# Optimization experiments

Hardware: AMD Instinct MI355X
Metric: run time of the kernel (lower is better)

The kernel has to match this reference:

```python
import jax, jax.numpy as jnp
import numpy as np

B, S, H = 8, 512, 768
NH, DH = 12, 64
I = 3072
E = 8
TOPK = 2
EPS = 1e-12


def _ln(x, g, b):
    m = jnp.mean(x, axis=-1, keepdims=True)
    v = jnp.mean(jnp.square(x - m), axis=-1, keepdims=True)
    return (x - m) * jax.lax.rsqrt(v + EPS) * g + b


def setup_inputs() -> dict:
    key = jax.random.key(0)
    ks = jax.random.split(key, 20)
    s_h = 1.0 / np.sqrt(H)
    s_i = 1.0 / np.sqrt(I)
    inp = {
        "hidden_states": jax.random.normal(ks[0], (B, S, H), jnp.float32),
        "Wq": jax.random.normal(ks[1], (H, H), jnp.float32) * s_h,
        "bq": jnp.zeros((H,), jnp.float32),
        "Wk": jax.random.normal(ks[2], (H, H), jnp.float32) * s_h,
        "bk": jnp.zeros((H,), jnp.float32),
        "Wv": jax.random.normal(ks[3], (H, H), jnp.float32) * s_h,
        "bv": jnp.zeros((H,), jnp.float32),
        "Wo": jax.random.normal(ks[4], (H, H), jnp.float32) * s_h,
        "bo": jnp.zeros((H,), jnp.float32),
        "ln_attn_g": jnp.ones((H,), jnp.float32),
        "ln_attn_b": jnp.zeros((H,), jnp.float32),
        "ln_ffn_g": jnp.ones((H,), jnp.float32),
        "ln_ffn_b": jnp.zeros((H,), jnp.float32),
        "Wr": jax.random.normal(ks[5], (H, E), jnp.float32) * s_h,
        "br": jnp.zeros((E,), jnp.float32),
        "W_up": jax.random.normal(ks[6], (E, H, I), jnp.float32) * s_h,
        "b_up": jnp.zeros((E, I), jnp.float32),
        "W_new": jax.random.normal(ks[7], (E, H, I), jnp.float32) * s_h,
        "b_new": jnp.zeros((E, I), jnp.float32),
        "W_down": jax.random.normal(ks[8], (E, I, H), jnp.float32) * s_i,
        "b_down": jnp.zeros((E, H), jnp.float32),
    }
    return inp


def reference(hidden_states, Wq, bq, Wk, bk, Wv, bv, Wo, bo,
              ln_attn_g, ln_attn_b, ln_ffn_g, ln_ffn_b,
              Wr, br, W_up, b_up, W_new, b_new, W_down, b_down):
    x = hidden_states
    # --- BertSelfAttention ---
    q = (x @ Wq + bq).reshape(B, S, NH, DH).transpose(0, 2, 1, 3)
    k = (x @ Wk + bk).reshape(B, S, NH, DH).transpose(0, 2, 1, 3)
    v = (x @ Wv + bv).reshape(B, S, NH, DH).transpose(0, 2, 1, 3)
    scores = jnp.einsum("bhqd,bhkd->bhqk", q, k) / np.sqrt(DH)
    probs = jax.nn.softmax(scores, axis=-1)
    ctx = jnp.einsum("bhqk,bhkd->bhqd", probs, v)
    ctx = ctx.transpose(0, 2, 1, 3).reshape(B, S, H)
    # --- BertSelfOutput: dense + residual + LayerNorm ---
    attention_output = _ln(ctx @ Wo + bo + x, ln_attn_g, ln_attn_b)
    # --- feed_forward_chunk: LayerNorm then token top-k MoE ---
    xl = _ln(attention_output, ln_ffn_g, ln_ffn_b)
    router_logits = xl @ Wr + br                      # [B,S,E]
    router_probs = jax.nn.softmax(router_logits, axis=-1)
    topw, topi = jax.lax.top_k(router_probs, TOPK)    # [B,S,K]
    topw = topw / jnp.sum(topw, axis=-1, keepdims=True)
    gates = jnp.sum(jax.nn.one_hot(topi, E, dtype=xl.dtype) * topw[..., None], axis=-2)  # [B,S,E]
    # --- experts (BertExpert: gelu(up(x)) * new(x) -> down), dense over E ---
    up = jax.nn.gelu(jnp.einsum("bsh,ehi->ebsi", xl, W_up) + b_up[:, None, None, :], approximate=False)
    gate_h = jnp.einsum("bsh,ehi->ebsi", xl, W_new) + b_new[:, None, None, :]
    y = jnp.einsum("ebsi,eih->ebsh", up * gate_h, W_down) + b_down[:, None, None, :]
    moe_out = jnp.einsum("ebsh,bse->bsh", y, gates)
    layer_output = moe_out + attention_output
    return layer_output, router_logits
```

## Files before the change

### kernel.cpp

```cpp
#include <hip/hip_runtime.h>
#include <hip/hip_bf16.h>
#include <cmath>


constexpr int cB = 8, cS = 512, cH = 768, cNH = 12, cDH = 64, cI = 3072, cE = 8;
constexpr int cT = cB * cS;
constexpr size_t TH = (size_t)cT * cH;

typedef __hip_bfloat16 bf16;
typedef __attribute__((ext_vector_type(8))) short s8v;
typedef __attribute__((ext_vector_type(4))) float f4v;

constexpr size_t SZ_WEXP     = (size_t)cE * cI * cH / 2;
constexpr size_t OFF_WUP_T   = 0;
constexpr size_t OFF_WNEW_T  = OFF_WUP_T + SZ_WEXP;
constexpr size_t OFF_WDOWN_T = OFF_WNEW_T + SZ_WEXP;
constexpr size_t OFF_QKV     = OFF_WDOWN_T + SZ_WEXP;
constexpr size_t OFF_CTX     = OFF_QKV + 4 * TH;
constexpr size_t OFF_XLB     = OFF_CTX + TH;
constexpr size_t OFF_WGT     = OFF_XLB + TH / 2;
constexpr size_t OFF_COUNTS  = OFF_WGT + 2 * cT;
constexpr size_t OFF_LISTS   = OFF_COUNTS + 16;

__device__ __forceinline__ void glds16(const void* g, void* l) {
    __builtin_amdgcn_global_load_lds(
        (const __attribute__((address_space(1))) unsigned int*)g,
        (__attribute__((address_space(3))) unsigned int*)l, 16, 0, 0);
}

__global__ void init_counts_kernel(int* __restrict__ counts) {
    if (threadIdx.x < cE) counts[threadIdx.x] = 0;
}

__global__ __launch_bounds__(256) void transpose_bf16_kernel(
    const float* __restrict__ src, bf16* __restrict__ dst, int R, int C) {
    __shared__ float tile[64][65];
    const size_t zb = (size_t)blockIdx.z * R * C;
    const int r0 = blockIdx.y * 64, c0 = blockIdx.x * 64;
    const int t = threadIdx.x;
    const int lr = t >> 4, lc = (t & 15) * 4;
#pragma unroll
    for (int i = 0; i < 4; ++i) {
        float4 v = *(const float4*)(src + zb + (size_t)(r0 + lr + i * 16) * C + c0 + lc);
        tile[lr + i * 16][lc + 0] = v.x; tile[lr + i * 16][lc + 1] = v.y;
        tile[lr + i * 16][lc + 2] = v.z; tile[lr + i * 16][lc + 3] = v.w;
    }
    __syncthreads();
#pragma unroll
    for (int i = 0; i < 4; ++i) {
        int cr = lr + i * 16;
        bf16 o[4];
#pragma unroll
        for (int j = 0; j < 4; ++j) o[j] = (bf16)tile[lc + j][cr];
        *(uint2*)(dst + zb + (size_t)(c0 + cr) * R + r0 + lc) = *(uint2*)o;
    }
}

__device__ __forceinline__ void gemm_body128(
    const float* __restrict__ A, const float* __restrict__ B,
    const float* __restrict__ bias, float* __restrict__ C,
    int N, int K, int m0, int n0) {
    __shared__ float As[16 * 132];
    __shared__ float Bs[16 * 128];
    const int t = threadIdx.x;
    const int tx = t & 15, ty = t >> 4;
    const int ar = t >> 2, ac = (t & 3) * 4;
    const int bc = (t & 31) * 4, br = t >> 5;
    const float* gB0 = B + (size_t)br * N + n0 + bc;
    float* dB0 = Bs + t * 4;
    float acc[8][8] = {};
    for (int k0 = 0; k0 < K; k0 += 16) {
        float4 a0 = *(const float4*)(A + (size_t)(m0 + ar) * K + k0 + ac);
        float4 a1 = *(const float4*)(A + (size_t)(m0 + ar + 64) * K + k0 + ac);
        glds16(gB0, dB0);
        glds16(gB0 + (size_t)8 * N, dB0 + 1024);
        As[(ac + 0) * 132 + ar] = a0.x; As[(ac + 1) * 132 + ar] = a0.y;
        As[(ac + 2) * 132 + ar] = a0.z; As[(ac + 3) * 132 + ar] = a0.w;
        As[(ac + 0) * 132 + ar + 64] = a1.x; As[(ac + 1) * 132 + ar + 64] = a1.y;
        As[(ac + 2) * 132 + ar + 64] = a1.z; As[(ac + 3) * 132 + ar + 64] = a1.w;
        __syncthreads();
#pragma unroll
        for (int kk = 0; kk < 16; ++kk) {
            float a[8], b[8];
            *(float4*)&a[0] = *(const float4*)&As[kk * 132 + ty * 8];
            *(float4*)&a[4] = *(const float4*)&As[kk * 132 + ty * 8 + 4];
            *(float4*)&b[0] = *(const float4*)&Bs[kk * 128 + tx * 4];
            *(float4*)&b[4] = *(const float4*)&Bs[kk * 128 + tx * 4 + 64];
#pragma unroll
            for (int i = 0; i < 8; ++i)
#pragma unroll
                for (int j = 0; j < 8; ++j) acc[i][j] += a[i] * b[j];
        }
        __syncthreads();
        gB0 += (size_t)16 * N;
    }
#pragma unroll
    for (int i = 0; i < 8; ++i) {
        int m = m0 + ty * 8 + i;
        float4 o0, o1;
        o0.x = acc[i][0] + bias[n0 + tx * 4 + 0];
        o0.y = acc[i][1] + bias[n0 + tx * 4 + 1];
        o0.z = acc[i][2] + bias[n0 + tx * 4 + 2];
        o0.w = acc[i][3] + bias[n0 + tx * 4 + 3];
        o1.x = acc[i][4] + bias[n0 + 64 + tx * 4 + 0];
        o1.y = acc[i][5] + bias[n0 + 64 + tx * 4 + 1];
        o1.z = acc[i][6] + bias[n0 + 64 + tx * 4 + 2];
        o1.w = acc[i][7] + bias[n0 + 64 + tx * 4 + 3];
        *(float4*)(C + (size_t)m * N + n0 + tx * 4) = o0;
        *(float4*)(C + (size_t)m * N + n0 + 64 + tx * 4) = o1;
    }
}

__global__ __launch_bounds__(256) void gemm_qkv_kernel(
    const float* __restrict__ A,
    const float* __restrict__ Wq, const float* __restrict__ Wk,
    const float* __restrict__ Wv,
    const float* __restrict__ bq, const float* __restrict__ bk,
    const float* __restrict__ bv,
    float* __restrict__ q, float* __restrict__ k, float* __restrict__ v) {
    const int z = blockIdx.z;
    const float* B = (z == 0) ? Wq : (z == 1) ? Wk : Wv;
    const float* bias = (z == 0) ? bq : (z == 1) ? bk : bv;
    float* C = (z == 0) ? q : (z == 1) ? k : v;
    gemm_body128(A, B, bias, C, cH, cH, blockIdx.y * 128, blockIdx.x * 128);
}

__global__ __launch_bounds__(256) void gemm_bias_kernel(
    const float* __restrict__ A, const float* __restrict__ B,
    const float* __restrict__ bias, float* __restrict__ C,
    int M, int N, int K) {
    gemm_body128(A, B, bias, C, N, K, blockIdx.y * 128, blockIdx.x * 128);
}

__global__ __launch_bounds__(256) void attn_kernel(
    const float* __restrict__ q, const float* __restrict__ k,
    const float* __restrict__ v, float* __restrict__ ctx) {
    __shared__ float sQ[64][68];
    __shared__ float sKV[64][68];
    __shared__ float sS[64][68];
    __shared__ float sM[64], sL[64], sAl[64];
    const int q0 = blockIdx.x * 64, h = blockIdx.y, b = blockIdx.z;
    const int t = threadIdx.x;
    const int lr = t >> 2, lq = (t & 3) * 16;
    {
        const float* gq = q + (size_t)(b * cS + q0 + lr) * cH + h * cDH + lq;
#pragma unroll
        for (int j = 0; j < 4; ++j) {
            float4 x = *(const float4*)(gq + j * 4);
            x.x *= 0.125f; x.y *= 0.125f; x.z *= 0.125f; x.w *= 0.125f;
            *(float4*)&sQ[lr][lq + j * 4] = x;
        }
    }
    if (t < 64) { sM[t] = -1e30f; sL[t] = 0.f; }
    const int c0 = t & 15, rr = (t >> 4) * 4;
    const int d4 = (t & 15) * 4, rp = (t >> 4) * 4;
    const int sr = t >> 2, sc = (t & 3) * 16;
    float4 o_acc[4];
#pragma unroll
    for (int i = 0; i < 4; ++i) o_acc[i] = make_float4(0.f, 0.f, 0.f, 0.f);

    for (int kt = 0; kt < 8; ++kt) {
        float4 kreg[4];
        {
            const float* gk = k + (size_t)(b * cS + kt * 64 + lr) * cH + h * cDH + lq;
#pragma unroll
            for (int j = 0; j < 4; ++j) kreg[j] = *(const float4*)(gk + j * 4);
        }
        __syncthreads();
#pragma unroll
        for (int j = 0; j < 4; ++j) *(float4*)&sKV[lr][lq + j * 4] = kreg[j];
        __syncthreads();
        float accS[4][4] = {};
#pragma unroll
        for (int d = 0; d < 64; d += 4) {
            float4 qv[4], kv[4];
#pragma unroll
            for (int i = 0; i < 4; ++i) qv[i] = *(const float4*)&sQ[rr + i][d];
#pragma unroll
            for (int j = 0; j < 4; ++j) kv[j] = *(const float4*)&sKV[c0 + 16 * j][d];
#pragma unroll
            for (int i = 0; i < 4; ++i)
#pragma unroll
                for (int j = 0; j < 4; ++j)
                    accS[i][j] += qv[i].x * kv[j].x + qv[i].y * kv[j].y +
                                  qv[i].z * kv[j].z + qv[i].w * kv[j].w;
        }
#pragma unroll
        for (int i = 0; i < 4; ++i)
#pragma unroll
            for (int j = 0; j < 4; ++j) sS[rr + i][c0 + 16 * j] = accS[i][j];
        float4 vreg[4];
        {
            const float* gv = v + (size_t)(b * cS + kt * 64 + lr) * cH + h * cDH + lq;
#pragma unroll
            for (int j = 0; j < 4; ++j) vreg[j] = *(const float4*)(gv + j * 4);
        }
        __syncthreads();
        {
            float4 s[4];
#pragma unroll
            for (int j = 0; j < 4; ++j) s[j] = *(const float4*)&sS[sr][sc + j * 4];
            float m = -1e30f;
#pragma unroll
            for (int j = 0; j < 4; ++j)
                m = fmaxf(m, fmaxf(fmaxf(s[j].x, s[j].y), fmaxf(s[j].z, s[j].w)));
            m = fmaxf(m, __shfl_xor(m, 1));
            m = fmaxf(m, __shfl_xor(m, 2));
            float m_old = sM[sr];
            float m_new = fmaxf(m_old, m);
            float sum = 0.f;
#pragma unroll
            for (int j = 0; j < 4; ++j) {
                s[j].x = __expf(s[j].x - m_new); s[j].y = __expf(s[j].y - m_new);
                s[j].z = __expf(s[j].z - m_new); s[j].w = __expf(s[j].w - m_new);
                sum += s[j].x + s[j].y + s[j].z + s[j].w;
                *(float4*)&sS[sr][sc + j * 4] = s[j];
            }
            sum += __shfl_xor(sum, 1);
            sum += __shfl_xor(sum, 2);
            if ((t & 3) == 0) {
                float alpha = __expf(m_old - m_new);
                sAl[sr] = alpha;
                sM[sr] = m_new;
                sL[sr] = sL[sr] * alpha + sum;
            }
        }
#pragma unroll
        for (int j = 0; j < 4; ++j) *(float4*)&sKV[lr][lq + j * 4] = vreg[j];
        __syncthreads();
#pragma unroll
        for (int i = 0; i < 4; ++i) {
            float al = sAl[rp + i];
            o_acc[i].x *= al; o_acc[i].y *= al; o_acc[i].z *= al; o_acc[i].w *= al;
        }
        for (int kk4 = 0; kk4 < 64; kk4 += 4) {
            float4 pv[4], vv[4];
#pragma unroll
            for (int i = 0; i < 4; ++i) pv[i] = *(const float4*)&sS[rp + i][kk4];
#pragma unroll
            for (int j = 0; j < 4; ++j) vv[j] = *(const float4*)&sKV[kk4 + j][d4];
#pragma unroll
            for (int i = 0; i < 4; ++i) {
                o_acc[i].x += pv[i].x * vv[0].x + pv[i].y * vv[1].x +
                              pv[i].z * vv[2].x + pv[i].w * vv[3].x;
                o_acc[i].y += pv[i].x * vv[0].y + pv[i].y * vv[1].y +
                              pv[i].z * vv[2].y + pv[i].w * vv[3].y;
                o_acc[i].z += pv[i].x * vv[0].z + pv[i].y * vv[1].z +
                              pv[i].z * vv[2].z + pv[i].w * vv[3].z;
                o_acc[i].w += pv[i].x * vv[0].w + pv[i].y * vv[1].w +
                              pv[i].z * vv[2].w + pv[i].w * vv[3].w;
            }
        }
    }
    __syncthreads();
#pragma unroll
    for (int i = 0; i < 4; ++i) {
        float inv = 1.0f / sL[rp + i];
        float4 o = o_acc[i];
        o.x *= inv; o.y *= inv; o.z *= inv; o.w *= inv;
        *(float4*)(ctx + (size_t)(b * cS + q0 + rp + i) * cH + h * cDH + d4) = o;
    }
}

__device__ __forceinline__ float block_reduce_sum(float v, float* red) {
#pragma unroll
    for (int o = 32; o; o >>= 1) v += __shfl_xor(v, o);
    __syncthreads();
    if ((threadIdx.x & 63) == 0) red[threadIdx.x >> 6] = v;
    __syncthreads();
    return red[0] + red[1] + red[2] + red[3];
}

__global__ __launch_bounds__(256) void ln_router_kernel(
    const float* __restrict__ dense, const float* __restrict__ resid,
    const float* __restrict__ g1, const float* __restrict__ b1,
    const float* __restrict__ g2, const float* __restrict__ b2,
    const float* __restrict__ Wr, const float* __restrict__ br,
    float* __restrict__ out, bf16* __restrict__ xlb,
    float* __restrict__ out_logits, float* __restrict__ wgt,
    int* __restrict__ counts, int* __restrict__ lists) {
    __shared__ float red[4];
    __shared__ float lred[4][8];
    const int t = blockIdx.x, tid = threadIdx.x;
    const size_t base = (size_t)t * cH;
    float v[3], s = 0.f;
#pragma unroll
    for (int i = 0; i < 3; ++i) {
        v[i] = dense[base + tid + 256 * i] + resid[base + tid + 256 * i];
        s += v[i];
    }
    const float mean = block_reduce_sum(s, red) * (1.0f / cH);
    float vs = 0.f;
#pragma unroll
    for (int i = 0; i < 3; ++i) { float d = v[i] - mean; vs += d * d; }
    const float rstd = rsqrtf(block_reduce_sum(vs, red) * (1.0f / cH) + 1e-12f);
    float a[3], s2 = 0.f;
#pragma unroll
    for (int i = 0; i < 3; ++i) {
        a[i] = (v[i] - mean) * rstd * g1[tid + 256 * i] + b1[tid + 256 * i];
        out[base + tid + 256 * i] = a[i];
        s2 += a[i];
    }
    const float mean2 = block_reduce_sum(s2, red) * (1.0f / cH);
    float vs2 = 0.f;
#pragma unroll
    for (int i = 0; i < 3; ++i) { float d = a[i] - mean2; vs2 += d * d; }
    const float rstd2 = rsqrtf(block_reduce_sum(vs2, red) * (1.0f / cH) + 1e-12f);
    float xl[3];
#pragma unroll
    for (int i = 0; i < 3; ++i) {
        xl[i] = (a[i] - mean2) * rstd2 * g2[tid + 256 * i] + b2[tid + 256 * i];
        xlb[base + tid + 256 * i] = (bf16)xl[i];
    }
    float lg[cE] = {};
#pragma unroll
    for (int i = 0; i < 3; ++i) {
        const float* wr = Wr + (size_t)(tid + 256 * i) * cE;
#pragma unroll
        for (int e = 0; e < cE; ++e) lg[e] += xl[i] * wr[e];
    }
#pragma unroll
    for (int e = 0; e < cE; ++e)
#pragma unroll
        for (int o = 32; o; o >>= 1) lg[e] += __shfl_xor(lg[e], o);
    if ((tid & 63) == 0)
#pragma unroll
        for (int e = 0; e < cE; ++e) lred[tid >> 6][e] = lg[e];
    __syncthreads();
    if (tid == 0) {
        float logits[cE];
#pragma unroll
        for (int e = 0; e < cE; ++e) {
            logits[e] = lred[0][e] + lred[1][e] + lred[2][e] + lred[3][e] + br[e];
            out_logits[(size_t)t * cE + e] = logits[e];
        }
        int i0 = 0;
        for (int e = 1; e < cE; ++e) if (logits[e] > logits[i0]) i0 = e;
        int i1 = (i0 == 0) ? 1 : 0;
        for (int e = 0; e < cE; ++e)
            if (e != i0 && logits[e] > logits[i1]) i1 = e;
        float e1 = __expf(logits[i1] - logits[i0]);
        float w0 = 1.0f / (1.0f + e1);
        float w1 = e1 * w0;
        wgt[t * 2 + 0] = w0;
        wgt[t * 2 + 1] = w1;
        int p0 = atomicAdd(&counts[i0], 1);
        lists[i0 * cT + p0] = t * 2 + 0;
        int p1 = atomicAdd(&counts[i1], 1);
        lists[i1 * cT + p1] = t * 2 + 1;
    }
}

__global__ __launch_bounds__(256) void expert_up_mfma_kernel(
    const bf16* __restrict__ xlb,
    const bf16* __restrict__ WupT, const bf16* __restrict__ WnewT,
    const float* __restrict__ b_up, const float* __restrict__ b_new,
    const int* __restrict__ counts, const int* __restrict__ lists,
    bf16* __restrict__ act) {
    const int e = blockIdx.z;
    const int cnt = counts[e];
    const int m0 = blockIdx.y * 128;
    if (m0 >= cnt) return;
    const int n0 = blockIdx.x * 64;
    __shared__ short sA[128 * 32], sB1[64 * 32], sB2[64 * 32];
    __shared__ int rowa[128];
    const int t = threadIdx.x;
    if (t < 128) {
        int idx = m0 + t;
        rowa[t] = (idx < cnt) ? lists[e * cT + idx] : -1;
    }
    __syncthreads();
    const int lane = t & 63, w = t >> 6;
    const int wm = (w >> 1) * 64, wn = (w & 1) * 32;
    const int rA0 = t >> 2, kc8 = (t & 3) * 8;
    int a0 = rowa[rA0], a1 = rowa[rA0 + 64];
    const bf16* gA0 = xlb + (size_t)(a0 < 0 ? 0 : (a0 >> 1)) * cH + kc8;
    const bf16* gA1 = xlb + (size_t)(a1 < 0 ? 0 : (a1 >> 1)) * cH + kc8;
    const bf16* B1 = WupT + (size_t)e * cI * cH;
    const bf16* B2 = WnewT + (size_t)e * cI * cH;
    const bf16* gB1 = B1 + (size_t)(n0 + rA0) * cH + kc8;
    const bf16* gB2 = B2 + (size_t)(n0 + rA0) * cH + kc8;
    short* dA0 = sA + t * 8;   short* dA1 = sA + (t + 256) * 8;
    short* dB1 = sB1 + t * 8;  short* dB2 = sB2 + t * 8;
    f4v zero = {0.f, 0.f, 0.f, 0.f};
    f4v acc1[4][2], acc2[4][2];
#pragma unroll
    for (int i = 0; i < 4; ++i)
#pragma unroll
        for (int j = 0; j < 2; ++j) { acc1[i][j] = zero; acc2[i][j] = zero; }
    const int fr = lane & 15, kg = (lane >> 4) * 8;
    for (int kk = 0; kk < cH; kk += 32) {
        glds16(gA0, dA0); glds16(gA1, dA1);
        glds16(gB1, dB1); glds16(gB2, dB2);
        __syncthreads();
        s8v af[4], bf1[2], bf2[2];
#pragma unroll
        for (int i = 0; i < 4; ++i)
            af[i] = *(const s8v*)(sA + (wm + i * 16 + fr) * 32 + kg);
#pragma unroll
        for (int j = 0; j < 2; ++j) {
            bf1[j] = *(const s8v*)(sB1 + (wn + j * 16 + fr) * 32 + kg);
            bf2[j] = *(const s8v*)(sB2 + (wn + j * 16 + fr) * 32 + kg);
        }
#pragma unroll
        for (int mi = 0; mi < 4; ++mi)
#pragma unroll
            for (int ni = 0; ni < 2; ++ni) {
                acc1[mi][ni] = __builtin_amdgcn_mfma_f32_16x16x32_bf16(
                    af[mi], bf1[ni], acc1[mi][ni], 0, 0, 0);
                acc2[mi][ni] = __builtin_amdgcn_mfma_f32_16x16x32_bf16(
                    af[mi], bf2[ni], acc2[mi][ni], 0, 0, 0);
            }
        __syncthreads();
        gA0 += 32; gA1 += 32; gB1 += 32; gB2 += 32;
    }
    const int cn = lane & 15, rq = (lane >> 4) * 4;
#pragma unroll
    for (int mi = 0; mi < 4; ++mi)
#pragma unroll
        for (int r = 0; r < 4; ++r) {
            int ml = wm + mi * 16 + rq + r;
            int a = rowa[ml];
            if (a < 0) continue;
            bf16* orow = act + (size_t)a * cI + n0 + wn;
#pragma unroll
            for (int ni = 0; ni < 2; ++ni) {
                int nl = ni * 16 + cn;
                float up = acc1[mi][ni][r] + b_up[e * cI + n0 + wn + nl];
                float nw = acc2[mi][ni][r] + b_new[e * cI + n0 + wn + nl];
                float g = 0.5f * up * (1.0f + erff(up * 0.70710678118654752f));
                orow[nl] = (bf16)(g * nw);
            }
        }
}

__global__ __launch_bounds__(256) void expert_down_mfma_kernel(
    const bf16* __restrict__ act, const bf16* __restrict__ WdownT,
    const float* __restrict__ b_down,
    const int* __restrict__ counts, const int* __restrict__ lists,
    const float* __restrict__ wgt, float* __restrict__ out) {
    const int e = blockIdx.z;
    const int cnt = counts[e];
    const int m0 = blockIdx.y * 128;
    if (m0 >= cnt) return;
    const int n0 = blockIdx.x * 128;
    __shared__ short sA[128 * 32], sB[128 * 32];
    __shared__ int rowa[128];
    const int t = threadIdx.x;
    if (t < 128) {
        int idx = m0 + t;
        rowa[t] = (idx < cnt) ? lists[e * cT + idx] : -1;
    }
    __syncthreads();
    const int lane = t & 63, w = t >> 6;
    const int wm = (w >> 1) * 64, wn = (w & 1) * 64;
    const int rA0 = t >> 2, kc8 = (t & 3) * 8;
    int a0 = rowa[rA0], a1 = rowa[rA0 + 64];
    const bf16* gA0 = act + (size_t)(a0 < 0 ? 0 : a0) * cI + kc8;
    const bf16* gA1 = act + (size_t)(a1 < 0 ? 0 : a1) * cI + kc8;
    const bf16* BT = WdownT + (size_t)e * cH * cI;
    const bf16* gB0 = BT + (size_t)(n0 + rA0) * cI + kc8;
    const bf16* gB1 = BT + (size_t)(n0 + rA0 + 64) * cI + kc8;
    short* dA0 = sA + t * 8;       short* dA1 = sA + (t + 256) * 8;
    short* dB0 = sB + t * 8;       short* dB1 = sB + (t + 256) * 8;
    f4v zero = {0.f, 0.f, 0.f, 0.f};
    f4v acc[4][4];
#pragma unroll
    for (int i = 0; i < 4; ++i)
#pragma unroll
        for (int j = 0; j < 4; ++j) acc[i][j] = zero;
    const int fr = lane & 15, kg = (lane >> 4) * 8;
    for (int kk = 0; kk < cI; kk += 32) {
        glds16(gA0, dA0); glds16(gA1, dA1);
        glds16(gB0, dB0); glds16(gB1, dB1);
        __syncthreads();
        s8v af[4], bf[4];
#pragma unroll
        for (int i = 0; i < 4; ++i) af[i] = *(const s8v*)(sA + (wm + i * 16 + fr) * 32 + kg);
#pragma unroll
        for (int i = 0; i < 4; ++i) bf[i] = *(const s8v*)(sB + (wn + i * 16 + fr) * 32 + kg);
#pragma unroll
        for (int mi = 0; mi < 4; ++mi)
#pragma unroll
            for (int ni = 0; ni < 4; ++ni)
                acc[mi][ni] = __builtin_amdgcn_mfma_f32_16x16x32_bf16(
                    af[mi], bf[ni], acc[mi][ni], 0, 0, 0);
        __syncthreads();
        gA0 += 32; gA1 += 32; gB0 += 32; gB1 += 32;
    }
    const int cn = lane & 15, rq = (lane >> 4) * 4;
#pragma unroll
    for (int mi = 0; mi < 4; ++mi)
#pragma unroll
        for (int r = 0; r < 4; ++r) {
            int ml = wm + mi * 16 + rq + r;
            int a = rowa[ml];
            if (a < 0) continue;
            int token = a >> 1;
            float wv = wgt[a];
#pragma unroll
            for (int ni = 0; ni < 4; ++ni) {
                int n = n0 + wn + ni * 16 + cn;
                atomicAdd(&out[(size_t)token * cH + n],
                          wv * (acc[mi][ni][r] + b_down[e * cH + n]));
            }
        }
}

extern "C" void kernel_launch(void* const* d_in, const int* in_sizes, int n_in,
                              void* d_out, int out_size, void* d_ws, size_t ws_size,
                              hipStream_t stream) {
    const float* x      = (const float*)d_in[0];
    const float* Wq     = (const float*)d_in[1];
    const float* bq     = (const float*)d_in[2];
    const float* Wk     = (const float*)d_in[3];
    const float* bk     = (const float*)d_in[4];
    const float* Wv     = (const float*)d_in[5];
    const float* bv     = (const float*)d_in[6];
    const float* Wo     = (const float*)d_in[7];
    const float* bo     = (const float*)d_in[8];
    const float* ln1g   = (const float*)d_in[9];
    const float* ln1b   = (const float*)d_in[10];
    const float* ln2g   = (const float*)d_in[11];
    const float* ln2b   = (const float*)d_in[12];
    const float* Wr     = (const float*)d_in[13];
    const float* br     = (const float*)d_in[14];
    const float* W_up   = (const float*)d_in[15];
    const float* b_up   = (const float*)d_in[16];
    const float* W_new  = (const float*)d_in[17];
    const float* b_new  = (const float*)d_in[18];
    const float* W_down = (const float*)d_in[19];
    const float* b_down = (const float*)d_in[20];

    float* out = (float*)d_out;
    float* ws  = (float*)d_ws;

    bf16* WupT   = (bf16*)(ws + OFF_WUP_T);
    bf16* WnewT  = (bf16*)(ws + OFF_WNEW_T);
    bf16* WdownT = (bf16*)(ws + OFF_WDOWN_T);
    float* q     = ws + OFF_QKV;
    float* k     = ws + OFF_QKV + TH;
    float* v     = ws + OFF_QKV + 2 * TH;
    float* tmp   = ws + OFF_QKV + 3 * TH;
    bf16* act    = (bf16*)(ws + OFF_QKV);
    float* ctx   = ws + OFF_CTX;
    bf16* xlb    = (bf16*)(ws + OFF_XLB);
    float* wgt   = ws + OFF_WGT;
    int* counts  = (int*)(ws + OFF_COUNTS);
    int* lists   = (int*)(ws + OFF_LISTS);

    init_counts_kernel<<<1, 64, 0, stream>>>(counts);

    transpose_bf16_kernel<<<dim3(48, 12, cE), 256, 0, stream>>>(W_up, WupT, cH, cI);
    transpose_bf16_kernel<<<dim3(48, 12, cE), 256, 0, stream>>>(W_new, WnewT, cH, cI);
    transpose_bf16_kernel<<<dim3(12, 48, cE), 256, 0, stream>>>(W_down, WdownT, cI, cH);

    gemm_qkv_kernel<<<dim3(cH / 128, cT / 128, 3), 256, 0, stream>>>(
        x, Wq, Wk, Wv, bq, bk, bv, q, k, v);
    attn_kernel<<<dim3(cS / 64, cNH, cB), 256, 0, stream>>>(q, k, v, ctx);
    gemm_bias_kernel<<<dim3(cH / 128, cT / 128), 256, 0, stream>>>(ctx, Wo, bo, tmp, cT, cH, cH);
    ln_router_kernel<<<cT, 256, 0, stream>>>(
        tmp, x, ln1g, ln1b, ln2g, ln2b, Wr, br,
        out, xlb, out + TH, wgt, counts, lists);

    expert_up_mfma_kernel<<<dim3(cI / 64, cT / 128, cE), 256, 0, stream>>>(
        xlb, WupT, WnewT, b_up, b_new, counts, lists, act);
    expert_down_mfma_kernel<<<dim3(cH / 128, cT / 128, cE), 256, 0, stream>>>(
        act, WdownT, b_down, counts, lists, wgt, out);
}
```

Baseline: 1.100 ms.

## Split-K the QKV and output-projection GEMMs with atomics and double-buffered LDS

The fp32 QKV projection is now split into two K halves and the output projection into four K quarters. Each slice accumulates into a pre-zeroed buffer with per-element atomicAdd, and only the first slice adds the bias. A zero kernel clears the q/k/v/tmp region first. The shared GEMM body also gains double-buffered LDS tiles that prefetch the next K step while computing the current one. The goal is to fill more CUs with a larger grid and to hide load latency, at the cost of scalar atomic traffic, an extra memset pass and nondeterministic summation order.

```diff
diff --git a/kernel.cpp b/kernel.cpp
--- a/kernel.cpp
+++ b/kernel.cpp
@@ -32,6 +32,13 @@
     if (threadIdx.x < cE) counts[threadIdx.x] = 0;
 }
 
+__global__ __launch_bounds__(256) void zero_kernel(float* __restrict__ p, int n4) {
+    float4 z = make_float4(0.f, 0.f, 0.f, 0.f);
+    for (int i = blockIdx.x * blockDim.x + threadIdx.x; i < n4;
+         i += gridDim.x * blockDim.x)
+        ((float4*)p)[i] = z;
+}
+
 __global__ __launch_bounds__(256) void transpose_bf16_kernel(
     const float* __restrict__ src, bf16* __restrict__ dst, int R, int C) {
     __shared__ float tile[64][65];
@@ -56,58 +63,80 @@
     }
 }
 
-__device__ __forceinline__ void gemm_body128(
+__device__ __forceinline__ void gemm_body128_ks(
     const float* __restrict__ A, const float* __restrict__ B,
     const float* __restrict__ bias, float* __restrict__ C,
-    int N, int K, int m0, int n0) {
-    __shared__ float As[16 * 132];
-    __shared__ float Bs[16 * 128];
+    int N, int K, int m0, int n0, int kbeg, int kend, bool addb) {
+    __shared__ float As[2][16 * 132];
+    __shared__ float Bs[2][16 * 128];
     const int t = threadIdx.x;
     const int tx = t & 15, ty = t >> 4;
     const int ar = t >> 2, ac = (t & 3) * 4;
-    const int bc = (t & 31) * 4, br = t >> 5;
-    const float* gB0 = B + (size_t)br * N + n0 + bc;
-    float* dB0 = Bs + t * 4;
+    const float* gB = B + (size_t)(t >> 5) * N + n0 + (t & 31) * 4;
     float acc[8][8] = {};
-    for (int k0 = 0; k0 < K; k0 += 16) {
-        float4 a0 = *(const float4*)(A + (size_t)(m0 + ar) * K + k0 + ac);
-        float4 a1 = *(const float4*)(A + (size_t)(m0 + ar + 64) * K + k0 + ac);
-        glds16(gB0, dB0);
-        glds16(gB0 + (size_t)8 * N, dB0 + 1024);
-        As[(ac + 0) * 132 + ar] = a0.x; As[(ac + 1) * 132 + ar] = a0.y;
-        As[(ac + 2) * 132 + ar] = a0.z; As[(ac + 3) * 132 + ar] = a0.w;
-        As[(ac + 0) * 132 + ar + 64] = a1.x; As[(ac + 1) * 132 + ar + 64] = a1.y;
-        As[(ac + 2) * 132 + ar + 64] = a1.z; As[(ac + 3) * 132 + ar + 64] = a1.w;
-        __syncthreads();
+
+    {
+        const float* g = gB + (size_t)kbeg * N;
+        float* d = &Bs[0][t * 4];
+        glds16(g, d);
+        glds16(g + (size_t)8 * N, d + 1024);
+        float4 a0 = *(const float4*)(A + (size_t)(m0 + ar) * K + kbeg + ac);
+        float4 a1 = *(const float4*)(A + (size_t)(m0 + ar + 64) * K + kbeg + ac);
+        As[0][(ac + 0) * 132 + ar] = a0.x; As[0][(ac + 1) * 132 + ar] = a0.y;
+        As[0][(ac + 2) * 132 + ar] = a0.z; As[0][(ac + 3) * 132 + ar] = a0.w;
+        As[0][(ac + 0) * 132 + ar + 64] = a1.x; As[0][(ac + 1) * 132 + ar + 64] = a1.y;
+        As[0][(ac + 2) * 132 + ar + 64] = a1.z; As[0][(ac + 3) * 132 + ar + 64] = a1.w;
+    }
+    __syncthreads();
+
+    int buf = 0;
+    for (int k0 = kbeg; k0 < kend; k0 += 16) {
+        const bool nxt = (k0 + 16) < kend;
+        float4 na0, na1;
+        if (nxt) {
+            const float* g = gB + (size_t)(k0 + 16) * N;
+            float* d = &Bs[buf ^ 1][t * 4];
+            glds16(g, d);
+            glds16(g + (size_t)8 * N, d + 1024);
+            na0 = *(const float4*)(A + (size_t)(m0 + ar) * K + k0 + 16 + ac);
+            na1 = *(const float4*)(A + (size_t)(m0 + ar + 64) * K + k0 + 16 + ac);
+        }
+        const float* Asb = &As[buf][0];
+        const float* Bsb = &Bs[buf][0];
 #pragma unroll
         for (int kk = 0; kk < 16; ++kk) {
             float a[8], b[8];
-            *(float4*)&a[0] = *(const float4*)&As[kk * 132 + ty * 8];
-            *(float4*)&a[4] = *(const float4*)&As[kk * 132 + ty * 8 + 4];
-            *(float4*)&b[0] = *(const float4*)&Bs[kk * 128 + tx * 4];
-            *(float4*)&b[4] = *(const float4*)&Bs[kk * 128 + tx * 4 + 64];
+            *(float4*)&a[0] = *(const float4*)&Asb[kk * 132 + ty * 8];
+            *(float4*)&a[4] = *(const float4*)&Asb[kk * 132 + ty * 8 + 4];
+            *(float4*)&b[0] = *(const float4*)&Bsb[kk * 128 + tx * 4];
+            *(float4*)&b[4] = *(const float4*)&Bsb[kk * 128 + tx * 4 + 64];
 #pragma unroll
             for (int i = 0; i < 8; ++i)
 #pragma unroll
                 for (int j = 0; j < 8; ++j) acc[i][j] += a[i] * b[j];
         }
-        __syncthreads();
-        gB0 += (size_t)16 * N;
-    }
+        if (nxt) {
+            float* s = &As[buf ^ 1][0];
+            s[(ac + 0) * 132 + ar] = na0.x; s[(ac + 1) * 132 + ar] = na0.y;
+            s[(ac + 2) * 132 + ar] = na0.z; s[(ac + 3) * 132 + ar] = na0.w;
+            s[(ac + 0) * 132 + ar + 64] = na1.x; s[(ac + 1) * 132 + ar + 64] = na1.y;
+            s[(ac + 2) * 132 + ar + 64] = na1.z; s[(ac + 3) * 132 + ar + 64] = na1.w;
+        }
+        __syncthreads();
+        buf ^= 1;
+    }
+
 #pragma unroll
     for (int i = 0; i < 8; ++i) {
         int m = m0 + ty * 8 + i;
-        float4 o0, o1;
-        o0.x = acc[i][0] + bias[n0 + tx * 4 + 0];
-        o0.y = acc[i][1] + bias[n0 + tx * 4 + 1];
-        o0.z = acc[i][2] + bias[n0 + tx * 4 + 2];
-        o0.w = acc[i][3] + bias[n0 + tx * 4 + 3];
-        o1.x = acc[i][4] + bias[n0 + 64 + tx * 4 + 0];
-        o1.y = acc[i][5] + bias[n0 + 64 + tx * 4 + 1];
-        o1.z = acc[i][6] + bias[n0 + 64 + tx * 4 + 2];
-        o1.w = acc[i][7] + bias[n0 + 64 + tx * 4 + 3];
-        *(float4*)(C + (size_t)m * N + n0 + tx * 4) = o0;
-        *(float4*)(C + (size_t)m * N + n0 + 64 + tx * 4) = o1;
+        float* cr = C + (size_t)m * N + n0;
+#pragma unroll
+        for (int j = 0; j < 4; ++j) {
+            float b0 = addb ? bias[n0 + tx * 4 + j] : 0.f;
+            float b1 = addb ? bias[n0 + 64 + tx * 4 + j] : 0.f;
+            atomicAdd(cr + tx * 4 + j, acc[i][j] + b0);
+            atomicAdd(cr + 64 + tx * 4 + j, acc[i][j + 4] + b1);
+        }
     }
 }
 
@@ -119,17 +148,22 @@
     const float* __restrict__ bv,
     float* __restrict__ q, float* __restrict__ k, float* __restrict__ v) {
     const int z = blockIdx.z;
-    const float* B = (z == 0) ? Wq : (z == 1) ? Wk : Wv;
-    const float* bias = (z == 0) ? bq : (z == 1) ? bk : bv;
-    float* C = (z == 0) ? q : (z == 1) ? k : v;
-    gemm_body128(A, B, bias, C, cH, cH, blockIdx.y * 128, blockIdx.x * 128);
+    const int p = z >> 1, ks = z & 1;
+    const float* B = (p == 0) ? Wq : (p == 1) ? Wk : Wv;
+    const float* bias = (p == 0) ? bq : (p == 1) ? bk : bv;
+    float* C = (p == 0) ? q : (p == 1) ? k : v;
+    gemm_body128_ks(A, B, bias, C, cH, cH, blockIdx.y * 128, blockIdx.x * 128,
+                    ks * 384, ks * 384 + 384, ks == 0);
 }
 
 __global__ __launch_bounds__(256) void gemm_bias_kernel(
     const float* __restrict__ A, const float* __restrict__ B,
     const float* __restrict__ bias, float* __restrict__ C,
     int M, int N, int K) {
-    gemm_body128(A, B, bias, C, N, K, blockIdx.y * 128, blockIdx.x * 128);
+    const int ks = blockIdx.z;
+    const int kq = K >> 2;
+    gemm_body128_ks(A, B, bias, C, N, K, blockIdx.y * 128, blockIdx.x * 128,
+                    ks * kq, ks * kq + kq, ks == 0);
 }
 
 __global__ __launch_bounds__(256) void attn_kernel(
@@ -550,15 +584,17 @@
     int* lists   = (int*)(ws + OFF_LISTS);
 
     init_counts_kernel<<<1, 64, 0, stream>>>(counts);
+    zero_kernel<<<2048, 256, 0, stream>>>(ws + OFF_QKV, (int)TH);
 
     transpose_bf16_kernel<<<dim3(48, 12, cE), 256, 0, stream>>>(W_up, WupT, cH, cI);
     transpose_bf16_kernel<<<dim3(48, 12, cE), 256, 0, stream>>>(W_new, WnewT, cH, cI);
     transpose_bf16_kernel<<<dim3(12, 48, cE), 256, 0, stream>>>(W_down, WdownT, cI, cH);
 
-    gemm_qkv_kernel<<<dim3(cH / 128, cT / 128, 3), 256, 0, stream>>>(
+    gemm_qkv_kernel<<<dim3(cH / 128, cT / 128, 6), 256, 0, stream>>>(
         x, Wq, Wk, Wv, bq, bk, bv, q, k, v);
     attn_kernel<<<dim3(cS / 64, cNH, cB), 256, 0, stream>>>(q, k, v, ctx);
-    gemm_bias_kernel<<<dim3(cH / 128, cT / 128), 256, 0, stream>>>(ctx, Wo, bo, tmp, cT, cH, cH);
+    gemm_bias_kernel<<<dim3(cH / 128, cT / 128, 4), 256, 0, stream>>>(
+        ctx, Wo, bo, tmp, cT, cH, cH);
     ln_router_kernel<<<cT, 256, 0, stream>>>(
         tmp, x, ln1g, ln1b, ln2g, ln2b, Wr, br,
         out, xlb, out + TH, wgt, counts, lists);
```

Result: slower. 1.428 ms (+29.9%).

## Shrink fp32 GEMM tiles to 64 rows and split-K the Wo projection

Applied to the files above, without the earlier changes.

Changes the shared fp32 SIMT GEMM body from 128x128 to 64x128 output tiles, doubling the number of blocks for the QKV and Wo projections. The Wo projection is additionally split in two along K, writing two partial outputs into the freed q/k buffers, and the LayerNorm/router kernel sums both partials with the residual. The aim is more blocks in flight on the many-CU GPU for these small GEMMs, in exchange for less register-level reuse per thread and an extra partial-sum buffer read in the LayerNorm.

```diff
diff --git a/kernel.cpp b/kernel.cpp
--- a/kernel.cpp
+++ b/kernel.cpp
@@ -56,38 +56,33 @@
     }
 }
 
-__device__ __forceinline__ void gemm_body128(
+__device__ __forceinline__ void gemm_body64(
     const float* __restrict__ A, const float* __restrict__ B,
     const float* __restrict__ bias, float* __restrict__ C,
-    int N, int K, int m0, int n0) {
-    __shared__ float As[16 * 132];
+    int N, int K, int m0, int n0, int kbeg, int kend, bool addb) {
+    __shared__ float As[16 * 68];
     __shared__ float Bs[16 * 128];
     const int t = threadIdx.x;
     const int tx = t & 15, ty = t >> 4;
     const int ar = t >> 2, ac = (t & 3) * 4;
-    const int bc = (t & 31) * 4, br = t >> 5;
-    const float* gB0 = B + (size_t)br * N + n0 + bc;
+    const float* gB0 = B + (size_t)kbeg * N + (size_t)(t >> 5) * N + n0 + (t & 31) * 4;
     float* dB0 = Bs + t * 4;
-    float acc[8][8] = {};
-    for (int k0 = 0; k0 < K; k0 += 16) {
+    float acc[4][8] = {};
+    for (int k0 = kbeg; k0 < kend; k0 += 16) {
         float4 a0 = *(const float4*)(A + (size_t)(m0 + ar) * K + k0 + ac);
-        float4 a1 = *(const float4*)(A + (size_t)(m0 + ar + 64) * K + k0 + ac);
         glds16(gB0, dB0);
         glds16(gB0 + (size_t)8 * N, dB0 + 1024);
-        As[(ac + 0) * 132 + ar] = a0.x; As[(ac + 1) * 132 + ar] = a0.y;
-        As[(ac + 2) * 132 + ar] = a0.z; As[(ac + 3) * 132 + ar] = a0.w;
-        As[(ac + 0) * 132 + ar + 64] = a1.x; As[(ac + 1) * 132 + ar + 64] = a1.y;
-        As[(ac + 2) * 132 + ar + 64] = a1.z; As[(ac + 3) * 132 + ar + 64] = a1.w;
+        As[(ac + 0) * 68 + ar] = a0.x; As[(ac + 1) * 68 + ar] = a0.y;
+        As[(ac + 2) * 68 + ar] = a0.z; As[(ac + 3) * 68 + ar] = a0.w;
         __syncthreads();
 #pragma unroll
         for (int kk = 0; kk < 16; ++kk) {
-            float a[8], b[8];
-            *(float4*)&a[0] = *(const float4*)&As[kk * 132 + ty * 8];
-            *(float4*)&a[4] = *(const float4*)&As[kk * 132 + ty * 8 + 4];
+            float a[4], b[8];
+            *(float4*)&a[0] = *(const float4*)&As[kk * 68 + ty * 4];
             *(float4*)&b[0] = *(const float4*)&Bs[kk * 128 + tx * 4];
             *(float4*)&b[4] = *(const float4*)&Bs[kk * 128 + tx * 4 + 64];
 #pragma unroll
-            for (int i = 0; i < 8; ++i)
+            for (int i = 0; i < 4; ++i)
 #pragma unroll
                 for (int j = 0; j < 8; ++j) acc[i][j] += a[i] * b[j];
         }
@@ -95,17 +90,17 @@
         gB0 += (size_t)16 * N;
     }
 #pragma unroll
-    for (int i = 0; i < 8; ++i) {
-        int m = m0 + ty * 8 + i;
+    for (int i = 0; i < 4; ++i) {
+        int m = m0 + ty * 4 + i;
         float4 o0, o1;
-        o0.x = acc[i][0] + bias[n0 + tx * 4 + 0];
-        o0.y = acc[i][1] + bias[n0 + tx * 4 + 1];
-        o0.z = acc[i][2] + bias[n0 + tx * 4 + 2];
-        o0.w = acc[i][3] + bias[n0 + tx * 4 + 3];
-        o1.x = acc[i][4] + bias[n0 + 64 + tx * 4 + 0];
-        o1.y = acc[i][5] + bias[n0 + 64 + tx * 4 + 1];
-        o1.z = acc[i][6] + bias[n0 + 64 + tx * 4 + 2];
-        o1.w = acc[i][7] + bias[n0 + 64 + tx * 4 + 3];
+        o0.x = acc[i][0]; o0.y = acc[i][1]; o0.z = acc[i][2]; o0.w = acc[i][3];
+        o1.x = acc[i][4]; o1.y = acc[i][5]; o1.z = acc[i][6]; o1.w = acc[i][7];
+        if (addb) {
+            o0.x += bias[n0 + tx * 4 + 0]; o0.y += bias[n0 + tx * 4 + 1];
+            o0.z += bias[n0 + tx * 4 + 2]; o0.w += bias[n0 + tx * 4 + 3];
+            o1.x += bias[n0 + 64 + tx * 4 + 0]; o1.y += bias[n0 + 64 + tx * 4 + 1];
+            o1.z += bias[n0 + 64 + tx * 4 + 2]; o1.w += bias[n0 + 64 + tx * 4 + 3];
+        }
         *(float4*)(C + (size_t)m * N + n0 + tx * 4) = o0;
         *(float4*)(C + (size_t)m * N + n0 + 64 + tx * 4) = o1;
     }
@@ -122,14 +117,18 @@
     const float* B = (z == 0) ? Wq : (z == 1) ? Wk : Wv;
     const float* bias = (z == 0) ? bq : (z == 1) ? bk : bv;
     float* C = (z == 0) ? q : (z == 1) ? k : v;
-    gemm_body128(A, B, bias, C, cH, cH, blockIdx.y * 128, blockIdx.x * 128);
-}
-
-__global__ __launch_bounds__(256) void gemm_bias_kernel(
-    const float* __restrict__ A, const float* __restrict__ B,
-    const float* __restrict__ bias, float* __restrict__ C,
-    int M, int N, int K) {
-    gemm_body128(A, B, bias, C, N, K, blockIdx.y * 128, blockIdx.x * 128);
+    gemm_body64(A, B, bias, C, cH, cH, blockIdx.y * 64, blockIdx.x * 128,
+                0, cH, true);
+}
+
+__global__ __launch_bounds__(256) void gemm_wo_kernel(
+    const float* __restrict__ A, const float* __restrict__ W,
+    const float* __restrict__ bias,
+    float* __restrict__ p0, float* __restrict__ p1) {
+    const int ks = blockIdx.z;
+    gemm_body64(A, W, bias, ks ? p1 : p0, cH, cH,
+                blockIdx.y * 64, blockIdx.x * 128,
+                ks * (cH / 2), ks * (cH / 2) + (cH / 2), ks == 0);
 }
 
 __global__ __launch_bounds__(256) void attn_kernel(
@@ -272,7 +271,8 @@
 }
 
 __global__ __launch_bounds__(256) void ln_router_kernel(
-    const float* __restrict__ dense, const float* __restrict__ resid,
+    const float* __restrict__ dense0, const float* __restrict__ dense1,
+    const float* __restrict__ resid,
     const float* __restrict__ g1, const float* __restrict__ b1,
     const float* __restrict__ g2, const float* __restrict__ b2,
     const float* __restrict__ Wr, const float* __restrict__ br,
@@ -286,7 +286,8 @@
     float v[3], s = 0.f;
 #pragma unroll
     for (int i = 0; i < 3; ++i) {
-        v[i] = dense[base + tid + 256 * i] + resid[base + tid + 256 * i];
+        v[i] = dense0[base + tid + 256 * i] + dense1[base + tid + 256 * i] +
+               resid[base + tid + 256 * i];
         s += v[i];
     }
     const float mean = block_reduce_sum(s, red) * (1.0f / cH);
@@ -555,12 +556,13 @@
     transpose_bf16_kernel<<<dim3(48, 12, cE), 256, 0, stream>>>(W_new, WnewT, cH, cI);
     transpose_bf16_kernel<<<dim3(12, 48, cE), 256, 0, stream>>>(W_down, WdownT, cI, cH);
 
-    gemm_qkv_kernel<<<dim3(cH / 128, cT / 128, 3), 256, 0, stream>>>(
+    gemm_qkv_kernel<<<dim3(cH / 128, cT / 64, 3), 256, 0, stream>>>(
         x, Wq, Wk, Wv, bq, bk, bv, q, k, v);
     attn_kernel<<<dim3(cS / 64, cNH, cB), 256, 0, stream>>>(q, k, v, ctx);
-    gemm_bias_kernel<<<dim3(cH / 128, cT / 128), 256, 0, stream>>>(ctx, Wo, bo, tmp, cT, cH, cH);
+    gemm_wo_kernel<<<dim3(cH / 128, cT / 64, 2), 256, 0, stream>>>(
+        ctx, Wo, bo, q, k);
     ln_router_kernel<<<cT, 256, 0, stream>>>(
-        tmp, x, ln1g, ln1b, ln2g, ln2b, Wr, br,
+        q, k, x, ln1g, ln1b, ln2g, ln2b, Wr, br,
         out, xlb, out + TH, wgt, counts, lists);
 
     expert_up_mfma_kernel<<<dim3(cI / 64, cT / 128, cE), 256, 0, stream>>>(
```

Result: faster. 1.052 ms (-4.4%).
